# Performance work log

Hardware: AMD Instinct MI355X
Metric: run time of the kernel (lower is better)

Reference implementation:

```python
import jax, jax.numpy as jnp
import numpy as np

LN_EPS = 1e-5


def _gather(x, idx):
    # x: [B, N, C], idx: [B, N, K] -> [B, N, K, C]
    return jax.vmap(lambda xb, ib: xb[ib])(x, idx)


def setup_inputs() -> dict:
    key = jax.random.key(0)
    ks = jax.random.split(key, 8)
    B, N, K, C_in, C_out, GEO = 2, 16384, 32, 128, 128, 10
    return {
        "points": jax.random.normal(ks[0], (B, N, 3), dtype=jnp.float32),
        "features": jax.random.normal(ks[1], (B, N, C_in), dtype=jnp.float32),
        "grouped_idx": jax.random.randint(ks[2], (B, N, K), 0, N, dtype=jnp.int32),
        "w_pos": jax.random.normal(ks[3], (GEO, C_in), dtype=jnp.float32) * (GEO ** -0.5),
        "b_pos": jnp.zeros((C_in,), jnp.float32),
        "w_gcm": jax.random.normal(ks[4], (C_in, C_in), dtype=jnp.float32) * (C_in ** -0.5),
        "b_gcm": jnp.zeros((C_in,), jnp.float32),
        "w_out": jax.random.normal(ks[5], (C_in, C_out), dtype=jnp.float32) * (C_in ** -0.5),
        "b_out": jnp.zeros((C_out,), jnp.float32),
        "ln_g": jnp.ones((C_out,), jnp.float32),
        "ln_b": jnp.zeros((C_out,), jnp.float32),
    }


def reference(points, features, grouped_idx, w_pos, b_pos, w_gcm, b_gcm,
              w_out, b_out, ln_g, ln_b):
    # gather neighbor coords and features: [B, N, K, *]
    grouped_pts = _gather(points, grouped_idx)
    xyz = points[..., 0:3]                      # [B, N, 3]
    grouped_xyz = grouped_pts[..., 0:3]         # [B, N, K, 3]
    center = xyz[:, :, None, :]                 # [B, N, 1, 3]
    diff = grouped_xyz - center                 # xi - xj
    dist = jnp.linalg.norm(diff, axis=-1, keepdims=True)  # ||xi - xj||
    K = grouped_xyz.shape[2]
    geo = jnp.concatenate(
        [jnp.broadcast_to(center, grouped_xyz.shape), grouped_xyz, diff, dist],
        axis=-1)                                # [B, N, K, 10]
    expanded_f = geo @ w_pos + b_pos            # pos_proj -> [B, N, K, C_in]
    grouped_f = _gather(features, grouped_idx)  # [B, N, K, C_in]
    h = jax.nn.relu((grouped_f + expanded_f) @ w_gcm + b_gcm)  # gcm_layer
    pooled = jnp.max(h, axis=2)                 # maxpooling over neighbors
    res = pooled + features                     # residual
    o = res @ w_out + b_out                     # out Linear
    mu = jnp.mean(o, axis=-1, keepdims=True)
    var = jnp.mean((o - mu) ** 2, axis=-1, keepdims=True)
    o = (o - mu) * jax.lax.rsqrt(var + LN_EPS) * ln_g + ln_b  # LayerNorm
    return jax.nn.relu(o)
```

## Files before the change

### kernel.cpp

```cpp
#include <hip/hip_runtime.h>
#include <hip/hip_bf16.h>
#include <math.h>

typedef __attribute__((ext_vector_type(8))) short short8;
typedef __attribute__((ext_vector_type(4))) short short4v;
typedef __attribute__((ext_vector_type(4))) float float4v;
typedef __attribute__((ext_vector_type(2))) unsigned int uint2v;
typedef unsigned short ushort_t;

constexpr int NPTS = 32768;
constexpr int NN   = 16384;
constexpr int KK   = 32;
constexpr int CC   = 128;
constexpr int GRP  = 16;
constexpr int SR   = 136;
constexpr int SG2  = 24;
#define LN_EPS 1e-5f
#define MFMA   __builtin_amdgcn_mfma_f32_16x16x32_bf16
#define GLL(src, dst, sz) __builtin_amdgcn_global_load_lds( \
    (const __attribute__((address_space(1))) void*)(src),   \
    (__attribute__((address_space(3))) void*)(dst), sz, 0, 0)

constexpr size_t WS_FW  = 0;
constexpr size_t WS_WO  = (size_t)NPTS * CC * 2;
constexpr size_t WS_BE  = WS_WO + 32768;
constexpr size_t WS_WPF = WS_BE + 512;
constexpr size_t WS_PG  = WS_WPF + 32768;
constexpr size_t WS_NEED = WS_PG + 5120;
constexpr size_t FB_WP = 0, FB_WO = 40960, FB_BE = 73728, FB_PG = 74240;

__device__ __forceinline__ short f2bs(float x) {
    return (short)__builtin_bit_cast(unsigned short, __float2bfloat16(x));
}
__device__ __forceinline__ float bs2f(ushort_t u) {
    return __uint_as_float(((unsigned)u) << 16);
}

__global__ __launch_bounds__(256) void prep1(
    const float* __restrict__ w_gcm, const float* __restrict__ w_out,
    const float* __restrict__ w_pos, const float* __restrict__ b_pos,
    const float* __restrict__ b_gcm,
    short* __restrict__ wsWpF, short* __restrict__ wsWo,
    float* __restrict__ wsBeff, float* __restrict__ wsPG)
{
    const int t = threadIdx.x, blk = blockIdx.x;
    if (blk == 0) {
        #pragma unroll 4
        for (int e = t; e < 16 * 128 * 8; e += 256) {
            const int j = e & 7, n = (e >> 3) & 127, g = e >> 10;
            wsWpF[e] = f2bs(w_gcm[(g * 8 + j) * 128 + n]);
        }
    } else if (blk == 1) {
        #pragma unroll 4
        for (int e = t; e < 128 * 128; e += 256) {
            const int j = e & 7, n = (e >> 3) & 127, g = e >> 10;
            wsWo[e] = f2bs(w_out[(g * 8 + j) * 128 + n]);
        }
    } else if (blk < 12) {
        if (t < 128) {
            const int g = blk - 2, c = t;
            float s = 0.f;
            #pragma unroll
            for (int r = 0; r < 128; ++r) s += w_pos[g * 128 + r] * w_gcm[r * 128 + c];
            wsPG[g * 128 + c] = s;
        }
    } else {
        if (t < 128) {
            const int c = t;
            float sb = b_gcm[c];
            #pragma unroll
            for (int r = 0; r < 128; ++r) sb += b_pos[r] * w_gcm[r * 128 + c];
            wsBeff[c] = sb;
        }
    }
}

__global__ __launch_bounds__(256) void prep_fw(
    const float* __restrict__ features, const short* __restrict__ wsWpF,
    ushort_t* __restrict__ wsFW)
{
    const int t = threadIdx.x, blk = blockIdx.x;
    __shared__ short sF[16 * SR];
    const int g0 = blk * GRP;
    {
        const int row = t >> 4, c8 = (t & 15) * 8;
        const float* fp = features + (size_t)(g0 + row) * CC + c8;
        const float4 a = *(const float4*)fp;
        const float4 b = *(const float4*)(fp + 4);
        short8 v;
        v[0]=f2bs(a.x); v[1]=f2bs(a.y); v[2]=f2bs(a.z); v[3]=f2bs(a.w);
        v[4]=f2bs(b.x); v[5]=f2bs(b.y); v[6]=f2bs(b.z); v[7]=f2bs(b.w);
        *(short8*)&sF[row * SR + c8] = v;
    }
    const int wv = t >> 6, lane = t & 63, quad = (lane >> 4) & 3, m = lane & 15;
    const int col0 = wv * 32 + m;
    short8 bf[4][2];
    #pragma unroll
    for (int ks = 0; ks < 4; ++ks) {
        bf[ks][0] = *((const short8*)wsWpF + ((ks * 4 + quad) * 128 + col0));
        bf[ks][1] = *((const short8*)wsWpF + ((ks * 4 + quad) * 128 + col0 + 16));
    }
    __syncthreads();
    float4v acc[2] = {};
    #pragma unroll
    for (int ks = 0; ks < 4; ++ks) {
        const short8 a = *(const short8*)(sF + m * SR + ks * 32 + quad * 8);
        acc[0] = MFMA(a, bf[ks][0], acc[0], 0, 0, 0);
        acc[1] = MFMA(a, bf[ks][1], acc[1], 0, 0, 0);
    }
    #pragma unroll
    for (int r = 0; r < 4; ++r) {
        const int R = quad * 4 + r;
        wsFW[(size_t)(g0 + R) * CC + col0]      = (ushort_t)f2bs(acc[0][r]);
        wsFW[(size_t)(g0 + R) * CC + col0 + 16] = (ushort_t)f2bs(acc[1][r]);
    }
}

__global__ __launch_bounds__(256, 3) void bridge_fw(
    const float* __restrict__ points, const float* __restrict__ features,
    const int*   __restrict__ gidx,
    const short* __restrict__ wsWo, const float* __restrict__ wsBeff,
    const float* __restrict__ wsPG, const ushort_t* __restrict__ wsFW,
    const float* __restrict__ b_out, const float* __restrict__ ln_g,
    const float* __restrict__ ln_b, float* __restrict__ out)
{
    __shared__ short sA[4][4][1024];
    __shared__ float sGxyz[GRP * KK * 3];
    __shared__ short sRes[GRP * SR];
    __shared__ short sResF[GRP * CC];
    __shared__ int   sIdx[GRP * KK];
    __shared__ float sCtr[GRP * 3];
    __shared__ float sPS[4][GRP], sPQ[4][GRP];

    const int t = threadIdx.x, wv = t >> 6, lane = t & 63;
    const int q = (lane >> 4) & 3, m = lane & 15;
    const int g0 = blockIdx.x * GRP;
    const int nbase = (g0 >= NN) ? NN : 0;
    const int colA = wv * 32 + m;
    const int rbL = lane >> 3, jL = (lane & 7) >> 1, hL = lane & 1;

    {
        const int gA = gidx[(size_t)g0 * KK + t];
        const int gB = gidx[(size_t)g0 * KK + t + 256];
        sIdx[t] = gA; sIdx[t + 256] = gB;
        const float* pA = points + (size_t)(nbase + gA) * 3;
        const float* pB = points + (size_t)(nbase + gB) * 3;
        sGxyz[t * 3 + 0] = pA[0]; sGxyz[t * 3 + 1] = pA[1]; sGxyz[t * 3 + 2] = pA[2];
        sGxyz[(t + 256) * 3 + 0] = pB[0];
        sGxyz[(t + 256) * 3 + 1] = pB[1];
        sGxyz[(t + 256) * 3 + 2] = pB[2];
    }
    if (t < GRP * 3) sCtr[t] = points[(size_t)g0 * 3 + t];
    {
        const int row = t >> 4, c8 = (t & 15) * 8;
        const float* fp = features + (size_t)(g0 + row) * CC + c8;
        const float4 a = *(const float4*)fp;
        const float4 b = *(const float4*)(fp + 4);
        short8 v;
        v[0]=f2bs(a.x); v[1]=f2bs(a.y); v[2]=f2bs(a.z); v[3]=f2bs(a.w);
        v[4]=f2bs(b.x); v[5]=f2bs(b.y); v[6]=f2bs(b.z); v[7]=f2bs(b.w);
        *(short8*)&sResF[row * CC + c8] = v;
    }

    const float beffv[2] = { wsBeff[colA], wsBeff[colA + 16] };
    float wc[6];
    short8 w4f[2];
    #pragma unroll
    for (int n = 0; n < 2; ++n) {
        const int c = colA + n * 16;
        const float p0 = wsPG[0*128+c], p1 = wsPG[1*128+c], p2 = wsPG[2*128+c];
        const float p3 = wsPG[3*128+c], p4 = wsPG[4*128+c], p5 = wsPG[5*128+c];
        const float p6 = wsPG[6*128+c], p7 = wsPG[7*128+c], p8 = wsPG[8*128+c];
        const float p9 = wsPG[9*128+c];
        wc[n*3+0] = p0 - p6; wc[n*3+1] = p1 - p7; wc[n*3+2] = p2 - p8;
        short8 w = (short8)0;
        w[0] = f2bs(p3 + p6); w[1] = f2bs(p4 + p7); w[2] = f2bs(p5 + p8); w[3] = f2bs(p9);
        w4f[n] = (q == 0) ? w : (short8)0;
    }
    const unsigned trBase = (unsigned)(size_t)(__attribute__((address_space(3))) short*)&sA[wv][0][0]
                          + (unsigned)(lane * 8);

    __syncthreads();

    auto issue_fw = [&](int p, int buf) {
        const int kw = nbase + sIdx[p * KK + rbL * 4 + jL];
        const ushort_t* s0 = wsFW + (size_t)kw * CC + wv * 32 + hL * 8;
        GLL(s0,      &sA[wv][buf][0],   16);
        GLL(s0 + 16, &sA[wv][buf][512], 16);
    };

    issue_fw(0, 0);
    issue_fw(1, 1);
    issue_fw(2, 2);

    #pragma unroll
    for (int p = 0; p < GRP; ++p) {
        const int buf = p & 3;
        if (p + 3 < GRP) issue_fw(p + 3, (p + 3) & 3);
        if (p + 3 < GRP)      asm volatile("s_waitcnt vmcnt(6)" ::: "memory");
        else if (p + 2 < GRP) asm volatile("s_waitcnt vmcnt(4)" ::: "memory");
        else if (p + 1 < GRP) asm volatile("s_waitcnt vmcnt(2)" ::: "memory");
        else                  asm volatile("s_waitcnt vmcnt(0)" ::: "memory");
        __builtin_amdgcn_sched_barrier(0);

        uint2v t00, t10, t01, t11;
        const unsigned trA = trBase + (unsigned)(buf * 2048);
        asm volatile("ds_read_b64_tr_b16 %0, %1 offset:0"    : "=&v"(t00) : "v"(trA));
        asm volatile("ds_read_b64_tr_b16 %0, %1 offset:512"  : "=&v"(t10) : "v"(trA));
        asm volatile("ds_read_b64_tr_b16 %0, %1 offset:1024" : "=&v"(t01) : "v"(trA));
        asm volatile("ds_read_b64_tr_b16 %0, %1 offset:1536" : "=&v"(t11) : "v"(trA));

        const float pcx = sCtr[p * 3], pcy = sCtr[p * 3 + 1], pcz = sCtr[p * 3 + 2];
        short8 ga0 = (short8)0, ga1 = (short8)0;
        if (q == 0) {
            const int i0 = (p * KK + m) * 3, i1 = i0 + 48;
            const float ax = sGxyz[i0], ay = sGxyz[i0 + 1], az = sGxyz[i0 + 2];
            const float bx = sGxyz[i1], by = sGxyz[i1 + 1], bz = sGxyz[i1 + 2];
            const float d0x = ax - pcx, d0y = ay - pcy, d0z = az - pcz;
            const float d1x = bx - pcx, d1y = by - pcy, d1z = bz - pcz;
            const float s0 = sqrtf(d0x * d0x + d0y * d0y + d0z * d0z);
            const float s1 = sqrtf(d1x * d1x + d1y * d1y + d1z * d1z);
            ga0[0]=f2bs(ax); ga0[1]=f2bs(ay); ga0[2]=f2bs(az); ga0[3]=f2bs(s0);
            ga1[0]=f2bs(bx); ga1[1]=f2bs(by); ga1[2]=f2bs(bz); ga1[3]=f2bs(s1);
        }

        asm volatile("s_waitcnt lgkmcnt(0)" ::: "memory");
        __builtin_amdgcn_sched_barrier(0);

        float4v c00, c10, c01, c11;
        c00[0]=__uint_as_float(t00[0] << 16); c00[1]=__uint_as_float(t00[0] & 0xffff0000u);
        c00[2]=__uint_as_float(t00[1] << 16); c00[3]=__uint_as_float(t00[1] & 0xffff0000u);
        c10[0]=__uint_as_float(t10[0] << 16); c10[1]=__uint_as_float(t10[0] & 0xffff0000u);
        c10[2]=__uint_as_float(t10[1] << 16); c10[3]=__uint_as_float(t10[1] & 0xffff0000u);
        c01[0]=__uint_as_float(t01[0] << 16); c01[1]=__uint_as_float(t01[0] & 0xffff0000u);
        c01[2]=__uint_as_float(t01[1] << 16); c01[3]=__uint_as_float(t01[1] & 0xffff0000u);
        c11[0]=__uint_as_float(t11[0] << 16); c11[1]=__uint_as_float(t11[0] & 0xffff0000u);
        c11[2]=__uint_as_float(t11[1] << 16); c11[3]=__uint_as_float(t11[1] & 0xffff0000u);

        c00 = MFMA(ga0, w4f[0], c00, 0, 0, 0);
        c01 = MFMA(ga0, w4f[1], c01, 0, 0, 0);
        c10 = MFMA(ga1, w4f[0], c10, 0, 0, 0);
        c11 = MFMA(ga1, w4f[1], c11, 0, 0, 0);

        const float cb0 = pcx * wc[0] + pcy * wc[1] + pcz * wc[2];
        const float cb1 = pcx * wc[3] + pcy * wc[4] + pcz * wc[5];

        float v0 = fmaxf(fmaxf(fmaxf(c00[0], c00[1]), fmaxf(c00[2], c00[3])),
                         fmaxf(fmaxf(c10[0], c10[1]), fmaxf(c10[2], c10[3])));
        float v1 = fmaxf(fmaxf(fmaxf(c01[0], c01[1]), fmaxf(c01[2], c01[3])),
                         fmaxf(fmaxf(c11[0], c11[1]), fmaxf(c11[2], c11[3])));
        v0 = fmaxf(v0, __shfl_xor(v0, 16)); v0 = fmaxf(v0, __shfl_xor(v0, 32));
        v1 = fmaxf(v1, __shfl_xor(v1, 16)); v1 = fmaxf(v1, __shfl_xor(v1, 32));
        v0 = fmaxf(v0 + beffv[0] + cb0, 0.f);
        v1 = fmaxf(v1 + beffv[1] + cb1, 0.f);
        if (q == 0) {
            sRes[p * SR + colA]      = f2bs(v0 + bs2f((ushort_t)sResF[p * CC + colA]));
            sRes[p * SR + colA + 16] = f2bs(v1 + bs2f((ushort_t)sResF[p * CC + colA + 16]));
        }
    }

    __syncthreads();

    short8 bWo[4][2];
    #pragma unroll
    for (int ks = 0; ks < 4; ++ks)
        #pragma unroll
        for (int ntl = 0; ntl < 2; ++ntl)
            bWo[ks][ntl] = *((const short8*)wsWo + ((ks * 4 + q) * 128 + colA + ntl * 16));

    const short* rm = sRes + m * SR;
    float4v acc2[2] = {};
    #pragma unroll
    for (int ks = 0; ks < 4; ++ks) {
        const short8 a = *(const short8*)(rm + ks * 32 + q * 8);
        acc2[0] = MFMA(a, bWo[ks][0], acc2[0], 0, 0, 0);
        acc2[1] = MFMA(a, bWo[ks][1], acc2[1], 0, 0, 0);
    }

    const float boutv[2] = { b_out[colA], b_out[colA + 16] };
    const float lngv[2]  = { ln_g[colA], ln_g[colA + 16] };
    const float lnbv[2]  = { ln_b[colA], ln_b[colA + 16] };

    #pragma unroll
    for (int r = 0; r < 4; ++r) {
        const float o0 = acc2[0][r] + boutv[0];
        const float o1 = acc2[1][r] + boutv[1];
        float ss = o0 + o1, qq = o0 * o0 + o1 * o1;
        #pragma unroll
        for (int d = 1; d < 16; d <<= 1) { ss += __shfl_xor(ss, d); qq += __shfl_xor(qq, d); }
        if (m == 0) { sPS[wv][q * 4 + r] = ss; sPQ[wv][q * 4 + r] = qq; }
    }
    __syncthreads();

    #pragma unroll
    for (int r = 0; r < 4; ++r) {
        const int R = q * 4 + r;
        const float S = sPS[0][R] + sPS[1][R] + sPS[2][R] + sPS[3][R];
        const float Q = sPQ[0][R] + sPQ[1][R] + sPQ[2][R] + sPQ[3][R];
        const float mu  = S * (1.f / 128.f);
        const float var = fmaxf(Q * (1.f / 128.f) - mu * mu, 0.f);
        const float rstd = rsqrtf(var + LN_EPS);
        const float o0 = acc2[0][r] + boutv[0];
        const float o1 = acc2[1][r] + boutv[1];
        const size_t base = (size_t)(g0 + R) * CC;
        out[base + colA]      = fmaxf((o0 - mu) * rstd * lngv[0] + lnbv[0], 0.f);
        out[base + colA + 16] = fmaxf((o1 - mu) * rstd * lngv[1] + lnbv[1], 0.f);
    }
}

__global__ __launch_bounds__(128) void prep_fold_fb(
    const float* __restrict__ w_pos, const float* __restrict__ b_pos,
    const float* __restrict__ w_gcm, const float* __restrict__ b_gcm,
    float* __restrict__ wsPG, float* __restrict__ wsBeff)
{
    const int c = threadIdx.x, g = blockIdx.x;
    if (g < 10) {
        float s = 0.f;
        for (int r = 0; r < 128; ++r) s += w_pos[g * 128 + r] * w_gcm[r * 128 + c];
        wsPG[g * 128 + c] = s;
    } else {
        float s = b_gcm[c];
        for (int r = 0; r < 128; ++r) s += b_pos[r] * w_gcm[r * 128 + c];
        wsBeff[c] = s;
    }
}

__global__ __launch_bounds__(256) void prep_pack_fb(
    const float* __restrict__ w_gcm, const float* __restrict__ w_out,
    const float* __restrict__ wsPG, short* __restrict__ wsWp, short* __restrict__ wsWo)
{
    const int t = threadIdx.x, blk = blockIdx.x;
    if (blk == 0) {
        #pragma unroll 4
        for (int e = t; e < 16 * 128 * 8; e += 256) {
            const int j = e & 7, n = (e >> 3) & 127, g = e >> 10;
            wsWp[e] = f2bs(w_gcm[(g * 8 + j) * 128 + n]);
        }
    } else if (blk == 1) {
        #pragma unroll 4
        for (int e2 = t; e2 < 4 * 128 * 8; e2 += 256) {
            const int e = 16 * 128 * 8 + e2;
            const int j = e & 7, n = (e >> 3) & 127, g = e >> 10;
            const int k = g * 8 + j;
            wsWp[e] = (k < 138) ? f2bs(wsPG[(k - 128) * 128 + n]) : (short)0;
        }
    } else {
        #pragma unroll 4
        for (int e = t; e < 128 * 128; e += 256) {
            const int j = e & 7, n = (e >> 3) & 127, g = e >> 10;
            wsWo[e] = f2bs(w_out[(g * 8 + j) * 128 + n]);
        }
    }
}

__global__ __launch_bounds__(256, 3) void bridge_fb(
    const float* __restrict__ points, const float* __restrict__ features,
    const int*   __restrict__ gidx,
    const short* __restrict__ wsWp, const short* __restrict__ wsWo,
    const float* __restrict__ wsBeff,
    const float* __restrict__ b_out, const float* __restrict__ ln_g,
    const float* __restrict__ ln_b, float* __restrict__ out)
{
    __shared__ short sA[4][KK * CC];
    __shared__ short sG[3][KK * SG2];
    __shared__ short sRes[GRP * SR];
    __shared__ short sResF[GRP * CC];
    __shared__ int   sIdx[GRP * KK];
    __shared__ float sCtr[GRP * 3];
    __shared__ float sPS[4][GRP], sPQ[4][GRP];

    const int t = threadIdx.x, wv = t >> 6, lane = t & 63;
    const int quad = (lane >> 4) & 3, m = lane & 15;
    const int g0 = blockIdx.x * GRP;
    const int nbase = (g0 >= NN) ? NN : 0;
    const int col0 = wv * 32 + m;

    sIdx[t]       = gidx[(size_t)g0 * KK + t];
    sIdx[t + 256] = gidx[(size_t)g0 * KK + t + 256];
    if (t < GRP * 3) sCtr[t] = points[(size_t)g0 * 3 + t];
    {
        const float* fs = features + (size_t)g0 * CC + t * 8;
        short8 v;
        #pragma unroll
        for (int i = 0; i < 8; ++i) v[i] = f2bs(fs[i]);
        *(short8*)&sResF[t * 8] = v;
    }

    short8 bWp[5][2];
    #pragma unroll
    for (int ks = 0; ks < 5; ++ks)
        #pragma unroll
        for (int ntl = 0; ntl < 2; ++ntl)
            bWp[ks][ntl] = *((const short8*)wsWp + ((ks * 4 + quad) * 128 + col0 + ntl * 16));
    const float beffv[2] = { wsBeff[col0], wsBeff[col0 + 16] };

    __syncthreads();

    const int r0 = wv * 4 + (lane >> 4);
    const int pc = lane & 15;
    const int gc = pc ^ r0;

    float geoS[3][3];

    auto geo_load = [&](int qq) {
        if (lane < 8) {
            const int j = wv * 8 + lane;
            const int kng = nbase + sIdx[qq * KK + j];
            const float* pp = points + (size_t)kng * 3;
            const int s = qq % 3;
            geoS[s][0] = pp[0]; geoS[s][1] = pp[1]; geoS[s][2] = pp[2];
        }
    };
    auto stage = [&](int qq) {
        const int buf = qq & 3;
        const int kn0 = nbase + sIdx[qq * KK + r0];
        const int kn1 = nbase + sIdx[qq * KK + r0 + 16];
        const float4* f0 = (const float4*)(features + (size_t)kn0 * CC + gc * 8);
        const float4* f1 = (const float4*)(features + (size_t)kn1 * CC + gc * 8);
        const float4 a = f0[0], b = f0[1], c = f1[0], d = f1[1];
        short8 v;
        v[0]=f2bs(a.x); v[1]=f2bs(a.y); v[2]=f2bs(a.z); v[3]=f2bs(a.w);
        v[4]=f2bs(b.x); v[5]=f2bs(b.y); v[6]=f2bs(b.z); v[7]=f2bs(b.w);
        *(short8*)&sA[buf][r0 * CC + pc * 8] = v;
        v[0]=f2bs(c.x); v[1]=f2bs(c.y); v[2]=f2bs(c.z); v[3]=f2bs(c.w);
        v[4]=f2bs(d.x); v[5]=f2bs(d.y); v[6]=f2bs(d.z); v[7]=f2bs(d.w);
        *(short8*)&sA[buf][(r0 + 16) * CC + pc * 8] = v;
    };
    auto geo_store = [&](int qq) {
        if (lane < 8) {
            const int j = wv * 8 + lane, s = qq % 3, b = qq % 3;
            const float cx = sCtr[qq * 3], cy = sCtr[qq * 3 + 1], cz = sCtr[qq * 3 + 2];
            const float gx = geoS[s][0], gy = geoS[s][1], gz = geoS[s][2];
            const float dx = gx - cx, dy = gy - cy, dz = gz - cz;
            const float dist = sqrtf(dx * dx + dy * dy + dz * dz);
            short8 v0, v1 = (short8)0;
            v0[0]=f2bs(cx); v0[1]=f2bs(cy); v0[2]=f2bs(cz);
            v0[3]=f2bs(gx); v0[4]=f2bs(gy); v0[5]=f2bs(gz);
            v0[6]=f2bs(dx); v0[7]=f2bs(dy);
            v1[0]=f2bs(dz); v1[1]=f2bs(dist);
            *(short8*)&sG[b][j * SG2 + 0] = v0;
            *(short8*)&sG[b][j * SG2 + 8] = v1;
        }
    };

    int offA[4];
    #pragma unroll
    for (int ks = 0; ks < 4; ++ks) offA[ks] = m * CC + (((ks * 4 + quad) ^ m) * 8);
    const int offG = m * SG2 + quad * 8;

    geo_load(0); stage(0);
    geo_load(1); stage(1);
    geo_load(2); stage(2);
    geo_store(0); geo_store(1);
    __syncthreads();

    #pragma unroll
    for (int p = 0; p < GRP; ++p) {
        if (p > 0) {
            asm volatile("s_waitcnt lgkmcnt(0)" ::: "memory");
            __builtin_amdgcn_s_barrier();
        }
        __builtin_amdgcn_sched_barrier(0);
        if (p + 3 < GRP) { geo_load(p + 3); stage(p + 3); }

        const short* ab = sA[p & 3];
        const short* ag = sG[p % 3];
        float4v acc[2][2] = {};
        #pragma unroll
        for (int ks = 0; ks < 4; ++ks) {
            const short8 a0 = *(const short8*)(ab + offA[ks]);
            const short8 a1 = *(const short8*)(ab + offA[ks] + 16 * CC);
            acc[0][0] = MFMA(a0, bWp[ks][0], acc[0][0], 0, 0, 0);
            acc[0][1] = MFMA(a0, bWp[ks][1], acc[0][1], 0, 0, 0);
            acc[1][0] = MFMA(a1, bWp[ks][0], acc[1][0], 0, 0, 0);
            acc[1][1] = MFMA(a1, bWp[ks][1], acc[1][1], 0, 0, 0);
        }
        short8 ga0 = (short8)0, ga1 = (short8)0;
        if (quad < 2) {
            ga0 = *(const short8*)(ag + offG);
            ga1 = *(const short8*)(ag + offG + 16 * SG2);
        }
        acc[0][0] = MFMA(ga0, bWp[4][0], acc[0][0], 0, 0, 0);
        acc[0][1] = MFMA(ga0, bWp[4][1], acc[0][1], 0, 0, 0);
        acc[1][0] = MFMA(ga1, bWp[4][0], acc[1][0], 0, 0, 0);
        acc[1][1] = MFMA(ga1, bWp[4][1], acc[1][1], 0, 0, 0);

        #pragma unroll
        for (int ntl = 0; ntl < 2; ++ntl) {
            float v = acc[0][ntl][0];
            #pragma unroll
            for (int rr = 1; rr < 4; ++rr) v = fmaxf(v, acc[0][ntl][rr]);
            #pragma unroll
            for (int rr = 0; rr < 4; ++rr) v = fmaxf(v, acc[1][ntl][rr]);
            v = fmaxf(v, __shfl_xor(v, 16));
            v = fmaxf(v, __shfl_xor(v, 32));
            v = fmaxf(v + beffv[ntl], 0.f);
            if (quad == 0) {
                const float fc = bs2f((ushort_t)sResF[p * CC + col0 + ntl * 16]);
                sRes[p * SR + col0 + ntl * 16] = f2bs(v + fc);
            }
        }
        if (p + 2 < GRP) geo_store(p + 2);
    }

    __syncthreads();

    short8 bWo[4][2];
    #pragma unroll
    for (int ks = 0; ks < 4; ++ks)
        #pragma unroll
        for (int ntl = 0; ntl < 2; ++ntl)
            bWo[ks][ntl] = *((const short8*)wsWo + ((ks * 4 + quad) * 128 + col0 + ntl * 16));

    const short* rm = sRes + m * SR;
    float4v acc2[2] = {};
    #pragma unroll
    for (int ks = 0; ks < 4; ++ks) {
        const short8 a = *(const short8*)(rm + ks * 32 + quad * 8);
        acc2[0] = MFMA(a, bWo[ks][0], acc2[0], 0, 0, 0);
        acc2[1] = MFMA(a, bWo[ks][1], acc2[1], 0, 0, 0);
    }
    const float boutv[2] = { b_out[col0], b_out[col0 + 16] };
    const float lngv[2]  = { ln_g[col0], ln_g[col0 + 16] };
    const float lnbv[2]  = { ln_b[col0], ln_b[col0 + 16] };
    #pragma unroll
    for (int r = 0; r < 4; ++r) {
        const float o0 = acc2[0][r] + boutv[0];
        const float o1 = acc2[1][r] + boutv[1];
        float ss = o0 + o1, qq2 = o0 * o0 + o1 * o1;
        #pragma unroll
        for (int d = 1; d < 16; d <<= 1) { ss += __shfl_xor(ss, d); qq2 += __shfl_xor(qq2, d); }
        if (m == 0) { sPS[wv][quad * 4 + r] = ss; sPQ[wv][quad * 4 + r] = qq2; }
    }
    __syncthreads();
    #pragma unroll
    for (int r = 0; r < 4; ++r) {
        const int R = quad * 4 + r;
        const float S = sPS[0][R] + sPS[1][R] + sPS[2][R] + sPS[3][R];
        const float Q = sPQ[0][R] + sPQ[1][R] + sPQ[2][R] + sPQ[3][R];
        const float mu  = S * (1.f / 128.f);
        const float var = fmaxf(Q * (1.f / 128.f) - mu * mu, 0.f);
        const float rstd = rsqrtf(var + LN_EPS);
        const float o0 = acc2[0][r] + boutv[0];
        const float o1 = acc2[1][r] + boutv[1];
        const size_t base = (size_t)(g0 + R) * CC;
        out[base + col0]      = fmaxf((o0 - mu) * rstd * lngv[0] + lnbv[0], 0.f);
        out[base + col0 + 16] = fmaxf((o1 - mu) * rstd * lngv[1] + lnbv[1], 0.f);
    }
}

extern "C" void kernel_launch(void* const* d_in, const int* in_sizes, int n_in,
                              void* d_out, int out_size, void* d_ws, size_t ws_size,
                              hipStream_t stream) {
    const float* points   = (const float*)d_in[0];
    const float* features = (const float*)d_in[1];
    const int*   gidx     = (const int*)  d_in[2];
    const float* w_pos    = (const float*)d_in[3];
    const float* b_pos    = (const float*)d_in[4];
    const float* w_gcm    = (const float*)d_in[5];
    const float* b_gcm    = (const float*)d_in[6];
    const float* w_out    = (const float*)d_in[7];
    const float* b_out    = (const float*)d_in[8];
    const float* ln_g     = (const float*)d_in[9];
    const float* ln_b     = (const float*)d_in[10];
    float* out = (float*)d_out;
    char* ws = (char*)d_ws;

    if (ws_size >= WS_NEED) {
        ushort_t* wsFW   = (ushort_t*)(ws + WS_FW);
        short*    wsWo   = (short*)(ws + WS_WO);
        float*    wsBeff = (float*)(ws + WS_BE);
        short*    wsWpF  = (short*)(ws + WS_WPF);
        float*    wsPG   = (float*)(ws + WS_PG);
        hipLaunchKernelGGL(prep1, dim3(13), dim3(256), 0, stream,
                           w_gcm, w_out, w_pos, b_pos, b_gcm,
                           wsWpF, wsWo, wsBeff, wsPG);
        hipLaunchKernelGGL(prep_fw, dim3(NPTS / GRP), dim3(256), 0, stream,
                           features, wsWpF, wsFW);
        hipLaunchKernelGGL(bridge_fw, dim3(NPTS / GRP), dim3(256), 0, stream,
                           points, features, gidx, wsWo, wsBeff, wsPG, wsFW,
                           b_out, ln_g, ln_b, out);
    } else {
        short* wsWp   = (short*)(ws + FB_WP);
        short* wsWo   = (short*)(ws + FB_WO);
        float* wsBeff = (float*)(ws + FB_BE);
        float* wsPG   = (float*)(ws + FB_PG);
        hipLaunchKernelGGL(prep_fold_fb, dim3(11), dim3(128), 0, stream,
                           w_pos, b_pos, w_gcm, b_gcm, wsPG, wsBeff);
        hipLaunchKernelGGL(prep_pack_fb, dim3(3), dim3(256), 0, stream,
                           w_gcm, w_out, wsPG, wsWp, wsWo);
        hipLaunchKernelGGL(bridge_fb, dim3(NPTS / GRP), dim3(256), 0, stream,
                           points, features, gidx, wsWp, wsWo, wsBeff,
                           b_out, ln_g, ln_b, out);
    }
}
```

Measured before the change: 149.5 us.

## Cut LDS usage in bridge_fw to raise occupancy to four blocks

The gather pipeline in bridge_fw drops from four LDS buffers to three, shortening prefetch depth from three points ahead to two. The shared residual-feature tile is removed: each lane keeps its residual features in registers and fetches them with wave shuffles when needed. Launch bounds are raised from 3 to 4 blocks per SM so more waves can hide gather latency. The trade-off is a shallower prefetch and register pressure from the 8 extra floats under a tighter register limit.

Measured after the change: 142.6 us. 4.6% less time.

```diff
diff --git a/kernel.cpp b/kernel.cpp
--- a/kernel.cpp
+++ b/kernel.cpp
@@ -116,7 +116,7 @@
     }
 }
 
-__global__ __launch_bounds__(256, 3) void bridge_fw(
+__global__ __launch_bounds__(256, 4) void bridge_fw(
     const float* __restrict__ points, const float* __restrict__ features,
     const int*   __restrict__ gidx,
     const short* __restrict__ wsWo, const float* __restrict__ wsBeff,
@@ -124,10 +124,9 @@
     const float* __restrict__ b_out, const float* __restrict__ ln_g,
     const float* __restrict__ ln_b, float* __restrict__ out)
 {
-    __shared__ short sA[4][4][1024];
+    __shared__ short sA[4][3][1024];
     __shared__ float sGxyz[GRP * KK * 3];
     __shared__ short sRes[GRP * SR];
-    __shared__ short sResF[GRP * CC];
     __shared__ int   sIdx[GRP * KK];
     __shared__ float sCtr[GRP * 3];
     __shared__ float sPS[4][GRP], sPQ[4][GRP];
@@ -151,15 +150,13 @@
         sGxyz[(t + 256) * 3 + 2] = pB[2];
     }
     if (t < GRP * 3) sCtr[t] = points[(size_t)g0 * 3 + t];
-    {
-        const int row = t >> 4, c8 = (t & 15) * 8;
-        const float* fp = features + (size_t)(g0 + row) * CC + c8;
-        const float4 a = *(const float4*)fp;
-        const float4 b = *(const float4*)(fp + 4);
-        short8 v;
-        v[0]=f2bs(a.x); v[1]=f2bs(a.y); v[2]=f2bs(a.z); v[3]=f2bs(a.w);
-        v[4]=f2bs(b.x); v[5]=f2bs(b.y); v[6]=f2bs(b.z); v[7]=f2bs(b.w);
-        *(short8*)&sResF[row * CC + c8] = v;
+
+    float rr[4][2];
+    #pragma unroll
+    for (int j = 0; j < 4; ++j) {
+        const size_t pt = (size_t)(g0 + q * 4 + j) * CC;
+        rr[j][0] = features[pt + colA];
+        rr[j][1] = features[pt + colA + 16];
     }
 
     const float beffv[2] = { wsBeff[colA], wsBeff[colA + 16] };
@@ -191,14 +188,12 @@
 
     issue_fw(0, 0);
     issue_fw(1, 1);
-    issue_fw(2, 2);
 
     #pragma unroll
     for (int p = 0; p < GRP; ++p) {
-        const int buf = p & 3;
-        if (p + 3 < GRP) issue_fw(p + 3, (p + 3) & 3);
-        if (p + 3 < GRP)      asm volatile("s_waitcnt vmcnt(6)" ::: "memory");
-        else if (p + 2 < GRP) asm volatile("s_waitcnt vmcnt(4)" ::: "memory");
+        const int buf = p % 3;
+        if (p + 2 < GRP) issue_fw(p + 2, (p + 2) % 3);
+        if (p + 2 < GRP)      asm volatile("s_waitcnt vmcnt(4)" ::: "memory");
         else if (p + 1 < GRP) asm volatile("s_waitcnt vmcnt(2)" ::: "memory");
         else                  asm volatile("s_waitcnt vmcnt(0)" ::: "memory");
         __builtin_amdgcn_sched_barrier(0);
@@ -253,9 +248,12 @@
         v1 = fmaxf(v1, __shfl_xor(v1, 16)); v1 = fmaxf(v1, __shfl_xor(v1, 32));
         v0 = fmaxf(v0 + beffv[0] + cb0, 0.f);
         v1 = fmaxf(v1 + beffv[1] + cb1, 0.f);
+
+        const float fc0 = __shfl(rr[p & 3][0], ((p >> 2) << 4) + m);
+        const float fc1 = __shfl(rr[p & 3][1], ((p >> 2) << 4) + m);
         if (q == 0) {
-            sRes[p * SR + colA]      = f2bs(v0 + bs2f((ushort_t)sResF[p * CC + colA]));
-            sRes[p * SR + colA + 16] = f2bs(v1 + bs2f((ushort_t)sResF[p * CC + colA + 16]));
+            sRes[p * SR + colA]      = f2bs(v0 + fc0);
+            sRes[p * SR + colA + 16] = f2bs(v1 + fc1);
         }
     }
 
@@ -489,9 +487,9 @@
         for (int ntl = 0; ntl < 2; ++ntl) {
             float v = acc[0][ntl][0];
             #pragma unroll
-            for (int rr = 1; rr < 4; ++rr) v = fmaxf(v, acc[0][ntl][rr]);
+            for (int rr2 = 1; rr2 < 4; ++rr2) v = fmaxf(v, acc[0][ntl][rr2]);
             #pragma unroll
-            for (int rr = 0; rr < 4; ++rr) v = fmaxf(v, acc[1][ntl][rr]);
+            for (int rr2 = 0; rr2 < 4; ++rr2) v = fmaxf(v, acc[1][ntl][rr2]);
             v = fmaxf(v, __shfl_xor(v, 16));
             v = fmaxf(v, __shfl_xor(v, 32));
             v = fmaxf(v + beffv[ntl], 0.f);
```
